# Kernel tuning notes

Hardware: AMD Instinct MI355X
Metric: run time of the kernel (lower is better)

The kernel has to match this reference:

```python
import jax, jax.numpy as jnp
import numpy as np

TOKENS = 8192
MODEL_DIM = 4096
PROMPT_DIM = 64
NUM_EXPERTS = 8
TOP_K = 2
EPS = float(np.finfo(np.float32).eps)


def setup_inputs() -> dict:
    key = jax.random.key(0)
    k1, k2, k3 = jax.random.split(key, 3)
    x = jax.random.normal(k1, (TOKENS, MODEL_DIM), dtype=jnp.float32)
    prompt = jax.random.normal(k2, (TOKENS, PROMPT_DIM), dtype=jnp.float32)
    # gate linear: Linear(model_dim + prompt_dim, num_experts, bias=True)
    W = jax.random.normal(k3, (MODEL_DIM + PROMPT_DIM, NUM_EXPERTS), dtype=jnp.float32) * 0.02
    b = jnp.zeros((NUM_EXPERTS,), dtype=jnp.float32)
    return {"x": x, "prompt": prompt, "W": W, "b": b}


def reference(x, prompt, W, b):
    # eval path: no jitter, no noise (self.training is False)
    logits = jnp.concatenate([x, prompt], axis=-1) @ W + b          # [T, E]
    _, topk_idx = jax.lax.top_k(logits, TOP_K)                      # [T, K]
    masks = jax.nn.one_hot(topk_idx, NUM_EXPERTS, dtype=jnp.float32)  # [T, K, E]
    gates = jax.nn.softmax(logits, axis=-1)                         # [T, E]
    gates_s = jnp.einsum("te,tke->tk", gates, masks)               # masked gather-sum
    if TOP_K > 1:
        denom = jnp.maximum(gates_s.sum(axis=-1, keepdims=True), EPS)
        gates_s = gates_s / denom
    # masks[:, i] == masks_se[i], gates_s[:, i] == gates_s[i] in the torch code
    return masks, gates_s
```

## Files before the change

### kernel.cpp

```cpp
#include <hip/hip_runtime.h>
#include <math.h>

#define NE 8
#define KDIM 4096
#define PDIM 64
#define WROWS (KDIM + PDIM)
#define EPS_F32 1.1920929e-07f

__global__ __launch_bounds__(256)
void transpose_w(const float* __restrict__ W, float* __restrict__ Wt) {
    const int k = blockIdx.x * 256 + threadIdx.x;
    if (k < WROWS) {
        float v[NE];
#pragma unroll
        for (int e = 0; e < NE; ++e) v[e] = W[(size_t)k * NE + e];
#pragma unroll
        for (int e = 0; e < NE; ++e) Wt[(size_t)e * WROWS + k] = v[e];
    }
}

__global__ __launch_bounds__(256, 4)
void topk_gate(const float* __restrict__ x,
               const float* __restrict__ prompt,
               const float* __restrict__ Wt,
               const float* __restrict__ b,
               float* __restrict__ out,
               int tokens)
{
    const int tid  = threadIdx.x;
    const int lane = tid & 63;
    const int ks   = tid >> 6;
    const int tblock = blockIdx.x * 4;

    __shared__ float lds[4][4][NE];

    float acc[4][NE];
#pragma unroll
    for (int t = 0; t < 4; ++t)
#pragma unroll
        for (int e = 0; e < NE; ++e) acc[t][e] = 0.f;

    const int kofs = ks * 1024;

#pragma unroll 2
    for (int i = 0; i < 4; ++i) {
        const int k = kofs + i * 256 + lane * 4;

        float4 xv[4];
#pragma unroll
        for (int t = 0; t < 4; ++t)
            xv[t] = *(const float4*)(x + (size_t)(tblock + t) * KDIM + k);

        float4 wv[NE];
#pragma unroll
        for (int e = 0; e < NE; ++e)
            wv[e] = *(const float4*)(Wt + (size_t)e * WROWS + k);

#pragma unroll
        for (int t = 0; t < 4; ++t)
#pragma unroll
            for (int e = 0; e < NE; ++e) {
                acc[t][e] = fmaf(xv[t].x, wv[e].x, acc[t][e]);
                acc[t][e] = fmaf(xv[t].y, wv[e].y, acc[t][e]);
                acc[t][e] = fmaf(xv[t].z, wv[e].z, acc[t][e]);
                acc[t][e] = fmaf(xv[t].w, wv[e].w, acc[t][e]);
            }
    }

    if (ks == 3 && lane < 16) {
        const int k = lane * 4;
        float4 pv[4];
#pragma unroll
        for (int t = 0; t < 4; ++t)
            pv[t] = *(const float4*)(prompt + (size_t)(tblock + t) * PDIM + k);
        float4 wv[NE];
#pragma unroll
        for (int e = 0; e < NE; ++e)
            wv[e] = *(const float4*)(Wt + (size_t)e * WROWS + KDIM + k);
#pragma unroll
        for (int t = 0; t < 4; ++t)
#pragma unroll
            for (int e = 0; e < NE; ++e) {
                acc[t][e] = fmaf(pv[t].x, wv[e].x, acc[t][e]);
                acc[t][e] = fmaf(pv[t].y, wv[e].y, acc[t][e]);
                acc[t][e] = fmaf(pv[t].z, wv[e].z, acc[t][e]);
                acc[t][e] = fmaf(pv[t].w, wv[e].w, acc[t][e]);
            }
    }

#pragma unroll
    for (int t = 0; t < 4; ++t)
#pragma unroll
        for (int e = 0; e < NE; ++e) {
            float v = acc[t][e];
#pragma unroll
            for (int off = 32; off >= 1; off >>= 1)
                v += __shfl_xor(v, off, 64);
            acc[t][e] = v;
        }

    if (lane < 32) {
        const int t = lane >> 3;
        const int e = lane & 7;
        lds[ks][t][e] = acc[t][e];
    }
    __syncthreads();

    if (tid < 64) {
        const int tl = tid >> 4;
        const int kk = (tid >> 3) & 1;
        const int ee = tid & 7;

        float lg[NE];
#pragma unroll
        for (int e = 0; e < NE; ++e)
            lg[e] = lds[0][tl][e] + lds[1][tl][e] + lds[2][tl][e] + lds[3][tl][e] + b[e];

        float v0 = lg[0]; int i0 = 0;
#pragma unroll
        for (int e = 1; e < NE; ++e)
            if (lg[e] > v0) { v0 = lg[e]; i0 = e; }
        float v1 = (i0 == 0) ? lg[1] : lg[0];
        int   i1 = (i0 == 0) ? 1 : 0;
#pragma unroll
        for (int e = 0; e < NE; ++e)
            if (e != i0 && lg[e] > v1) { v1 = lg[e]; i1 = e; }

        float s = 0.f;
#pragma unroll
        for (int e = 0; e < NE; ++e) s += __expf(lg[e] - v0);
        const float g0 = 1.0f / s;
        const float g1 = __expf(v1 - v0) / s;
        const float denom = fmaxf(g0 + g1, EPS_F32);

        const int t_global = tblock + tl;
        const int sel = kk ? i1 : i0;
        out[(size_t)t_global * 16 + kk * 8 + ee] = (ee == sel) ? 1.0f : 0.0f;

        if ((tid & 15) < 2) {
            const float g = (ee == 0) ? (g0 / denom) : (g1 / denom);
            out[(size_t)tokens * 16 + (size_t)t_global * 2 + ee] = g;
        }
    }
}

extern "C" void kernel_launch(void* const* d_in, const int* in_sizes, int n_in,
                              void* d_out, int out_size, void* d_ws, size_t ws_size,
                              hipStream_t stream) {
    const float* x      = (const float*)d_in[0];
    const float* prompt = (const float*)d_in[1];
    const float* W      = (const float*)d_in[2];
    const float* b      = (const float*)d_in[3];
    float* out          = (float*)d_out;
    float* Wt           = (float*)d_ws;

    const int tokens = in_sizes[0] / KDIM;

    hipLaunchKernelGGL(transpose_w, dim3((WROWS + 255) / 256), dim3(256), 0, stream,
                       W, Wt);
    hipLaunchKernelGGL(topk_gate, dim3(tokens / 4), dim3(256), 0, stream,
                       x, prompt, Wt, b, out, tokens);
}
```

Baseline: 226.6 us.

## Use single-wave blocks with register-pipelined K loop and no LDS reduction

Each block becomes a single 64-lane wavefront that walks the whole K dimension for 4 tokens. It software-pipelines the x and W loads through a 3-deep register buffer and uses nontemporal loads for x. This removes the cross-wave LDS reduction and the __syncthreads. The cost is much higher register pressure (buffers of 3x12 float4) and 4x fewer threads per block, which may reduce latency hiding if occupancy drops.

```diff
diff --git a/kernel.cpp b/kernel.cpp
--- a/kernel.cpp
+++ b/kernel.cpp
@@ -6,6 +6,10 @@
 #define PDIM 64
 #define WROWS (KDIM + PDIM)
 #define EPS_F32 1.1920929e-07f
+#define NCHUNK 16
+#define DEPTH 3
+
+typedef float f4 __attribute__((ext_vector_type(4)));
 
 __global__ __launch_bounds__(256)
 void transpose_w(const float* __restrict__ W, float* __restrict__ Wt) {
@@ -19,7 +23,7 @@
     }
 }
 
-__global__ __launch_bounds__(256, 4)
+__global__ __launch_bounds__(64, 2)
 void topk_gate(const float* __restrict__ x,
                const float* __restrict__ prompt,
                const float* __restrict__ Wt,
@@ -27,12 +31,9 @@
                float* __restrict__ out,
                int tokens)
 {
-    const int tid  = threadIdx.x;
-    const int lane = tid & 63;
-    const int ks   = tid >> 6;
-    const int tblock = blockIdx.x * 4;
-
-    __shared__ float lds[4][4][NE];
+    const int lane  = threadIdx.x;
+    const int tbase = blockIdx.x * 4;
+    const int klane = lane * 4;
 
     float acc[4][NE];
 #pragma unroll
@@ -40,43 +41,48 @@
 #pragma unroll
         for (int e = 0; e < NE; ++e) acc[t][e] = 0.f;
 
-    const int kofs = ks * 1024;
+    f4 xb[DEPTH][4];
+    f4 wb[DEPTH][NE];
 
-#pragma unroll 2
-    for (int i = 0; i < 4; ++i) {
-        const int k = kofs + i * 256 + lane * 4;
-
-        float4 xv[4];
+    auto load_chunk = [&](int c, int s) {
+        const int k = c * 256 + klane;
 #pragma unroll
         for (int t = 0; t < 4; ++t)
-            xv[t] = *(const float4*)(x + (size_t)(tblock + t) * KDIM + k);
-
-        float4 wv[NE];
+            xb[s][t] = __builtin_nontemporal_load(
+                (const f4*)(x + (size_t)(tbase + t) * KDIM + k));
 #pragma unroll
         for (int e = 0; e < NE; ++e)
-            wv[e] = *(const float4*)(Wt + (size_t)e * WROWS + k);
+            wb[s][e] = *(const f4*)(Wt + (size_t)e * WROWS + k);
+    };
 
+    load_chunk(0, 0);
+    load_chunk(1, 1);
+
+#pragma unroll
+    for (int c = 0; c < NCHUNK; ++c) {
+        if (c + 2 < NCHUNK) load_chunk(c + 2, (c + 2) % DEPTH);
+        const int s = c % DEPTH;
 #pragma unroll
         for (int t = 0; t < 4; ++t)
 #pragma unroll
             for (int e = 0; e < NE; ++e) {
-                acc[t][e] = fmaf(xv[t].x, wv[e].x, acc[t][e]);
-                acc[t][e] = fmaf(xv[t].y, wv[e].y, acc[t][e]);
-                acc[t][e] = fmaf(xv[t].z, wv[e].z, acc[t][e]);
-                acc[t][e] = fmaf(xv[t].w, wv[e].w, acc[t][e]);
+                acc[t][e] = fmaf(xb[s][t].x, wb[s][e].x, acc[t][e]);
+                acc[t][e] = fmaf(xb[s][t].y, wb[s][e].y, acc[t][e]);
+                acc[t][e] = fmaf(xb[s][t].z, wb[s][e].z, acc[t][e]);
+                acc[t][e] = fmaf(xb[s][t].w, wb[s][e].w, acc[t][e]);
             }
     }
 
-    if (ks == 3 && lane < 16) {
+    if (lane < 16) {
         const int k = lane * 4;
-        float4 pv[4];
+        f4 pv[4];
 #pragma unroll
         for (int t = 0; t < 4; ++t)
-            pv[t] = *(const float4*)(prompt + (size_t)(tblock + t) * PDIM + k);
-        float4 wv[NE];
+            pv[t] = *(const f4*)(prompt + (size_t)(tbase + t) * PDIM + k);
+        f4 wv[NE];
 #pragma unroll
         for (int e = 0; e < NE; ++e)
-            wv[e] = *(const float4*)(Wt + (size_t)e * WROWS + KDIM + k);
+            wv[e] = *(const f4*)(Wt + (size_t)e * WROWS + KDIM + k);
 #pragma unroll
         for (int t = 0; t < 4; ++t)
 #pragma unroll
@@ -99,48 +105,44 @@
             acc[t][e] = v;
         }
 
-    if (lane < 32) {
-        const int t = lane >> 3;
-        const int e = lane & 7;
-        lds[ks][t][e] = acc[t][e];
+    const int tt = lane >> 4;
+    const int kk = (lane >> 3) & 1;
+    const int ee = lane & 7;
+
+    float lg[NE];
+#pragma unroll
+    for (int e = 0; e < NE; ++e) {
+        float v = acc[0][e];
+        if (tt == 1) v = acc[1][e];
+        if (tt == 2) v = acc[2][e];
+        if (tt == 3) v = acc[3][e];
+        lg[e] = v + b[e];
     }
-    __syncthreads();
 
-    if (tid < 64) {
-        const int tl = tid >> 4;
-        const int kk = (tid >> 3) & 1;
-        const int ee = tid & 7;
+    float v0 = lg[0]; int i0 = 0;
+#pragma unroll
+    for (int e = 1; e < NE; ++e)
+        if (lg[e] > v0) { v0 = lg[e]; i0 = e; }
+    float v1 = (i0 == 0) ? lg[1] : lg[0];
+    int   i1 = (i0 == 0) ? 1 : 0;
+#pragma unroll
+    for (int e = 0; e < NE; ++e)
+        if (e != i0 && lg[e] > v1) { v1 = lg[e]; i1 = e; }
 
-        float lg[NE];
+    float s = 0.f;
 #pragma unroll
-        for (int e = 0; e < NE; ++e)
-            lg[e] = lds[0][tl][e] + lds[1][tl][e] + lds[2][tl][e] + lds[3][tl][e] + b[e];
+    for (int e = 0; e < NE; ++e) s += __expf(lg[e] - v0);
+    const float g0 = 1.0f / s;
+    const float g1 = __expf(v1 - v0) / s;
+    const float denom = fmaxf(g0 + g1, EPS_F32);
 
-        float v0 = lg[0]; int i0 = 0;
-#pragma unroll
-        for (int e = 1; e < NE; ++e)
-            if (lg[e] > v0) { v0 = lg[e]; i0 = e; }
-        float v1 = (i0 == 0) ? lg[1] : lg[0];
-        int   i1 = (i0 == 0) ? 1 : 0;
-#pragma unroll
-        for (int e = 0; e < NE; ++e)
-            if (e != i0 && lg[e] > v1) { v1 = lg[e]; i1 = e; }
+    const int sel = kk ? i1 : i0;
+    const int t_global = tbase + tt;
+    out[(size_t)t_global * 16 + kk * 8 + ee] = (ee == sel) ? 1.0f : 0.0f;
 
-        float s = 0.f;
-#pragma unroll
-        for (int e = 0; e < NE; ++e) s += __expf(lg[e] - v0);
-        const float g0 = 1.0f / s;
-        const float g1 = __expf(v1 - v0) / s;
-        const float denom = fmaxf(g0 + g1, EPS_F32);
-
-        const int t_global = tblock + tl;
-        const int sel = kk ? i1 : i0;
-        out[(size_t)t_global * 16 + kk * 8 + ee] = (ee == sel) ? 1.0f : 0.0f;
-
-        if ((tid & 15) < 2) {
-            const float g = (ee == 0) ? (g0 / denom) : (g1 / denom);
-            out[(size_t)tokens * 16 + (size_t)t_global * 2 + ee] = g;
-        }
+    if ((lane & 15) < 2) {
+        const float g = (ee == 0) ? (g0 / denom) : (g1 / denom);
+        out[(size_t)tokens * 16 + (size_t)t_global * 2 + ee] = g;
     }
 }
 
@@ -158,6 +160,6 @@
 
     hipLaunchKernelGGL(transpose_w, dim3((WROWS + 255) / 256), dim3(256), 0, stream,
                        W, Wt);
-    hipLaunchKernelGGL(topk_gate, dim3(tokens / 4), dim3(256), 0, stream,
+    hipLaunchKernelGGL(topk_gate, dim3(tokens / 4), dim3(64), 0, stream,
                        x, prompt, Wt, b, out, tokens);
 }
```

After: 209.1 us. 7.7% less time.
